# Optimization experiments

Hardware: AMD Instinct MI355X
Metric: run time of the kernel (lower is better)

Reference implementation:

```python
import jax, jax.numpy as jnp
import numpy as np

INPUTDIM = 256
OUTDIM = 256
GRIDSIZE = 300


def setup_inputs() -> dict:
    key = jax.random.key(0)
    k1, k2 = jax.random.split(key)
    x = jax.random.normal(k1, (1024, INPUTDIM), dtype=jnp.float32)
    scale = 1.0 / (np.sqrt(INPUTDIM) * np.sqrt(GRIDSIZE))
    fouriercoeffs = jax.random.normal(k2, (2, OUTDIM, INPUTDIM, GRIDSIZE), dtype=jnp.float32) * scale
    bias = jnp.zeros((1, OUTDIM), dtype=jnp.float32)
    return {"x": x, "fouriercoeffs": fouriercoeffs, "bias": bias}


def reference(x, fouriercoeffs, bias):
    # x: (B, I); fouriercoeffs: (2, O, I, G); bias: (1, O)
    outshape = x.shape[:-1] + (OUTDIM,)
    xf = x.reshape(-1, INPUTDIM)
    k = jnp.arange(1, GRIDSIZE + 1, dtype=xf.dtype)  # (G,)
    phase = xf[:, :, None] * k[None, None, :]        # (B, I, G)
    c = jnp.cos(phase)
    s = jnp.sin(phase)
    y = jnp.einsum('big,jig->bj', c, fouriercoeffs[0]) \
        + jnp.einsum('big,jig->bj', s, fouriercoeffs[1])
    y = y + bias
    return y.reshape(outshape)
```

## Files before the change

kernel.cpp:

```cpp
#include <hip/hip_runtime.h>

#define BATCH   1024
#define IDIM    256
#define ODIM    256
#define GRIDSZ  300

#define BM      128
#define BN      128
#define MT      8
#define NT      2
#define KS_     64
#define IPW     4
#define GS_STEPS 19
#define NSTEPS  (IPW*GS_STEPS)
#define AP      40
#define INV2PI  0.15915494309189535f

typedef __attribute__((ext_vector_type(8))) short  short8;
typedef __attribute__((ext_vector_type(4))) float  f32x4;
typedef __attribute__((ext_vector_type(4))) unsigned int u32x4;

__device__ __forceinline__ unsigned pk(float c, float s) {
  unsigned a = __float_as_uint(c) + 0x8000u;
  unsigned b = __float_as_uint(s) + 0x8000u;
  return __builtin_amdgcn_perm(b, a, 0x07060302u);
}

__device__ __forceinline__ void rot(float& c, float& s, float C, float S) {
  float t1 = s * S;
  float t2 = c * S;
  float cn = __builtin_fmaf(c, C, -t1);
  s = __builtin_fmaf(s, C, t2);
  c = cn;
}

__device__ __forceinline__ void cossin(float rev, float& c, float& s) {
  c = __builtin_amdgcn_cosf(__builtin_amdgcn_fractf(rev));
  s = __builtin_amdgcn_cosf(__builtin_amdgcn_fractf(rev - 0.25f));
}

__global__ void init_out(const float* __restrict__ bias, float* __restrict__ out) {
  const int idx = blockIdx.x * 256 + threadIdx.x;
  out[idx] = bias[idx & (ODIM - 1)];
}

__global__ __launch_bounds__(256, 3) void fkan_gemm(
    const float* __restrict__ x, const float* __restrict__ fc,
    float* __restrict__ out) {
  __shared__ alignas(16) short A_lds[BM * AP];
  __shared__ alignas(16) short B_lds[BN * AP];

  const int tid = threadIdx.x;
  const int id  = blockIdx.x;
  const int z = id & 7, q = id >> 3;
  const int m = q & 7, r = q >> 3;
  const int n  = z & 1;
  const int ks = (z >> 1) | (r << 2);

  const int wave = tid >> 6, lane = tid & 63;
  const int wm = wave >> 1, wn = wave & 1;
  const int fr = lane & 15, fq = lane >> 4;

  const int rA = tid >> 1;
  const int hB = tid & 1;

  const float* xrow = x + (size_t)(m * BM + rA) * IDIM + ks * IPW;
  const float* b0 = fc + ((size_t)(n * BN + rA) * IDIM + ks * IPW) * GRIDSZ + hB * 8;
  const float* b1 = b0 + (size_t)ODIM * IDIM * GRIDSZ;

  short* Awr = &A_lds[rA * AP + hB * 16];
  short* Bwr = &B_lds[rA * AP + hB * 16];
  const short* Ard = &A_lds[(wm * 64 + fr) * AP + fq * 8];
  const short* Brd = &B_lds[(wn * 64 + fr) * AP + fq * 8];

  f32x4 acc[4][4];
#pragma unroll
  for (int a_ = 0; a_ < 4; ++a_)
#pragma unroll
    for (int b_ = 0; b_ < 4; ++b_)
      acc[a_][b_] = (f32x4){0.f, 0.f, 0.f, 0.f};

  float xr = xrow[0] * INV2PI;
  float r1c, r1s, r16c, r16s, sc, ss;
  cossin(xr, r1c, r1s);
  cossin(xr * 16.0f, r16c, r16s);
  cossin(xr * (float)(hB * 8 + 1), sc, ss);
  unsigned ad[8];
  {
    float c = sc, s = ss;
    ad[0] = pk(c, s);
#pragma unroll
    for (int u = 1; u < 8; ++u) { rot(c, s, r1c, r1s); ad[u] = pk(c, s); }
  }
  unsigned bw[8];
  {
    f32x4 L0a = *(const f32x4*)(b0);
    f32x4 L0b = *(const f32x4*)(b0 + 4);
    f32x4 L1a = *(const f32x4*)(b1);
    f32x4 L1b = *(const f32x4*)(b1 + 4);
    bw[0] = pk(L0a.x, L1a.x); bw[1] = pk(L0a.y, L1a.y);
    bw[2] = pk(L0a.z, L1a.z); bw[3] = pk(L0a.w, L1a.w);
    bw[4] = pk(L0b.x, L1b.x); bw[5] = pk(L0b.y, L1b.y);
    bw[6] = pk(L0b.z, L1b.z); bw[7] = pk(L0b.w, L1b.w);
  }

  int il = 0, gs = 0, soff = 0;

  for (int S = 0; S < NSTEPS; ++S) {
    *(u32x4*)Awr       = (u32x4){ad[0], ad[1], ad[2], ad[3]};
    *(u32x4*)(Awr + 8) = (u32x4){ad[4], ad[5], ad[6], ad[7]};
    *(u32x4*)Bwr       = (u32x4){bw[0], bw[1], bw[2], bw[3]};
    *(u32x4*)(Bwr + 8) = (u32x4){bw[4], bw[5], bw[6], bw[7]};
    __syncthreads();

    int gsn = gs + 1, iln = il;
    if (gsn == GS_STEPS) { gsn = 0; iln++; }
    const bool newil = (gsn == 0);
    if (iln >= IPW) iln = 0;
    const int soffn = newil ? iln * GRIDSZ : soff + 16;
    const int o2 = soffn + ((((gsn == 18) ? 1 : 0) & hB) ? 0 : 4);
    f32x4 L0a = *(const f32x4*)(b0 + soffn);
    f32x4 L0b = *(const f32x4*)(b0 + o2);
    f32x4 L1a = *(const f32x4*)(b1 + soffn);
    f32x4 L1b = *(const f32x4*)(b1 + o2);

    short8 aF[4];
#pragma unroll
    for (int tI = 0; tI < 4; ++tI) aF[tI] = *(const short8*)(Ard + tI * 16 * AP);
#pragma unroll
    for (int tJ = 0; tJ < 4; ++tJ) {
      short8 bF = *(const short8*)(Brd + tJ * 16 * AP);
#pragma unroll
      for (int tI = 0; tI < 4; ++tI)
        acc[tI][tJ] = __builtin_amdgcn_mfma_f32_16x16x32_bf16(aF[tI], bF, acc[tI][tJ], 0, 0, 0);
    }

    if (newil) {
      xr = xrow[iln] * INV2PI;
      cossin(xr, r1c, r1s);
      cossin(xr * 16.0f, r16c, r16s);
      cossin(xr * (float)(hB * 8 + 1), sc, ss);
    } else {
      rot(sc, ss, r16c, r16s);
    }
    {
      float c = sc, s = ss;
      ad[0] = pk(c, s);
#pragma unroll
      for (int u = 1; u < 8; ++u) { rot(c, s, r1c, r1s); ad[u] = pk(c, s); }
    }
    if (((gsn == 18) ? 1 : 0) & hB) { ad[4] = 0u; ad[5] = 0u; ad[6] = 0u; ad[7] = 0u; }

    bw[0] = pk(L0a.x, L1a.x); bw[1] = pk(L0a.y, L1a.y);
    bw[2] = pk(L0a.z, L1a.z); bw[3] = pk(L0a.w, L1a.w);
    bw[4] = pk(L0b.x, L1b.x); bw[5] = pk(L0b.y, L1b.y);
    bw[6] = pk(L0b.z, L1b.z); bw[7] = pk(L0b.w, L1b.w);

    il = iln; gs = gsn; soff = soffn;
    __syncthreads();
  }

  const int ob = m * BM + wm * 64 + fq * 4;
  const int oj = n * BN + wn * 64 + fr;
#pragma unroll
  for (int tI = 0; tI < 4; ++tI)
#pragma unroll
    for (int tJ = 0; tJ < 4; ++tJ) {
      float* dst = out + (size_t)(ob + tI * 16) * ODIM + (oj + tJ * 16);
#pragma unroll
      for (int rr = 0; rr < 4; ++rr)
        unsafeAtomicAdd(dst + rr * ODIM, acc[tI][tJ][rr]);
    }
}

extern "C" void kernel_launch(void* const* d_in, const int* in_sizes, int n_in,
                              void* d_out, int out_size, void* d_ws, size_t ws_size,
                              hipStream_t stream) {
  const float* x    = (const float*)d_in[0];
  const float* fc   = (const float*)d_in[1];
  const float* bias = (const float*)d_in[2];
  float* out = (float*)d_out;

  init_out<<<dim3(BATCH * ODIM / 256), dim3(256), 0, stream>>>(bias, out);
  fkan_gemm<<<dim3(MT * NT * KS_), dim3(256), 0, stream>>>(x, fc, out);
}
```

Measured before the change: 367.8 us.

## Halve M tile and double-buffer LDS with a single barrier per step

Shrinks the batch tile from 128 to 64 rows, doubling the grid and halving per-wave accumulators and A-side trig work, with launch bounds raised to 5 blocks per CU. LDS is double-buffered so each step writes the next tile into the other half while MFMAs consume the current one, dropping one of the two barriers per step. The aim is more occupancy and better overlap of global loads and sincos generation with matrix work. In exchange, B-tile loads and output atomics double in total, since each B tile is now shared by fewer batch rows.

```diff
diff --git a/kernel.cpp b/kernel.cpp
--- a/kernel.cpp
+++ b/kernel.cpp
@@ -5,15 +5,17 @@
 #define ODIM    256
 #define GRIDSZ  300
 
-#define BM      128
+#define BM      64
 #define BN      128
-#define MT      8
+#define MT      16
 #define NT      2
 #define KS_     64
 #define IPW     4
 #define GS_STEPS 19
 #define NSTEPS  (IPW*GS_STEPS)
 #define AP      40
+#define B_OFF   2560
+#define HALF_LDS 7680
 #define INV2PI  0.15915494309189535f
 
 typedef __attribute__((ext_vector_type(8))) short  short8;
@@ -44,102 +46,110 @@
   out[idx] = bias[idx & (ODIM - 1)];
 }
 
-__global__ __launch_bounds__(256, 3) void fkan_gemm(
+__global__ __launch_bounds__(256, 5) void fkan_gemm(
     const float* __restrict__ x, const float* __restrict__ fc,
     float* __restrict__ out) {
-  __shared__ alignas(16) short A_lds[BM * AP];
-  __shared__ alignas(16) short B_lds[BN * AP];
+  __shared__ alignas(16) short lds[2 * HALF_LDS];
 
   const int tid = threadIdx.x;
   const int id  = blockIdx.x;
   const int z = id & 7, q = id >> 3;
-  const int m = q & 7, r = q >> 3;
-  const int n  = z & 1;
-  const int ks = (z >> 1) | (r << 2);
+  const int m = q & 15, w = q >> 4;
+  const int c_ = (w << 3) | z;
+  const int ks = c_ >> 1, n = c_ & 1;
 
   const int wave = tid >> 6, lane = tid & 63;
   const int wm = wave >> 1, wn = wave & 1;
   const int fr = lane & 15, fq = lane >> 4;
 
-  const int rA = tid >> 1;
-  const int hB = tid & 1;
+  const int rowA = tid >> 2, q8 = tid & 3;
+  const int rowB = tid >> 1, hB = tid & 1;
 
-  const float* xrow = x + (size_t)(m * BM + rA) * IDIM + ks * IPW;
-  const float* b0 = fc + ((size_t)(n * BN + rA) * IDIM + ks * IPW) * GRIDSZ + hB * 8;
+  const float* xrow = x + (size_t)(m * BM + rowA) * IDIM + ks * IPW;
+  const float* b0 = fc + ((size_t)(n * BN + rowB) * IDIM + ks * IPW) * GRIDSZ;
   const float* b1 = b0 + (size_t)ODIM * IDIM * GRIDSZ;
 
-  short* Awr = &A_lds[rA * AP + hB * 16];
-  short* Bwr = &B_lds[rA * AP + hB * 16];
-  const short* Ard = &A_lds[(wm * 64 + fr) * AP + fq * 8];
-  const short* Brd = &B_lds[(wn * 64 + fr) * AP + fq * 8];
+  const int AwrO = rowA * AP + q8 * 8;
+  const int BwrO = B_OFF + rowB * AP + hB * 16;
+  const int ArdO = (wm * 32 + fr) * AP + fq * 8;
+  const int BrdO = B_OFF + (wn * 64 + fr) * AP + fq * 8;
 
-  f32x4 acc[4][4];
+  f32x4 acc[2][4];
 #pragma unroll
-  for (int a_ = 0; a_ < 4; ++a_)
+  for (int a_ = 0; a_ < 2; ++a_)
 #pragma unroll
     for (int b_ = 0; b_ < 4; ++b_)
       acc[a_][b_] = (f32x4){0.f, 0.f, 0.f, 0.f};
 
-  float xr = xrow[0] * INV2PI;
-  float r1c, r1s, r16c, r16s, sc, ss;
+  float r1c, r1s, r16c, r16s, sc, ss, xr;
+  xr = xrow[0] * INV2PI;
   cossin(xr, r1c, r1s);
-  cossin(xr * 16.0f, r16c, r16s);
-  cossin(xr * (float)(hB * 8 + 1), sc, ss);
-  unsigned ad[8];
+  cossin(16.0f * xr, r16c, r16s);
+  cossin((float)(q8 * 4 + 1) * xr, sc, ss);
+
+  unsigned ad[4];
   {
     float c = sc, s = ss;
     ad[0] = pk(c, s);
 #pragma unroll
-    for (int u = 1; u < 8; ++u) { rot(c, s, r1c, r1s); ad[u] = pk(c, s); }
+    for (int u = 1; u < 4; ++u) { rot(c, s, r1c, r1s); ad[u] = pk(c, s); }
   }
   unsigned bw[8];
   {
-    f32x4 L0a = *(const f32x4*)(b0);
-    f32x4 L0b = *(const f32x4*)(b0 + 4);
-    f32x4 L1a = *(const f32x4*)(b1);
-    f32x4 L1b = *(const f32x4*)(b1 + 4);
+    const int gb = hB * 8;
+    f32x4 L0a = *(const f32x4*)(b0 + gb);
+    f32x4 L0b = *(const f32x4*)(b0 + gb + 4);
+    f32x4 L1a = *(const f32x4*)(b1 + gb);
+    f32x4 L1b = *(const f32x4*)(b1 + gb + 4);
     bw[0] = pk(L0a.x, L1a.x); bw[1] = pk(L0a.y, L1a.y);
     bw[2] = pk(L0a.z, L1a.z); bw[3] = pk(L0a.w, L1a.w);
     bw[4] = pk(L0b.x, L1b.x); bw[5] = pk(L0b.y, L1b.y);
     bw[6] = pk(L0b.z, L1b.z); bw[7] = pk(L0b.w, L1b.w);
   }
+  *(u32x4*)&lds[AwrO]     = (u32x4){ad[0], ad[1], ad[2], ad[3]};
+  *(u32x4*)&lds[BwrO]     = (u32x4){bw[0], bw[1], bw[2], bw[3]};
+  *(u32x4*)&lds[BwrO + 8] = (u32x4){bw[4], bw[5], bw[6], bw[7]};
 
   int il = 0, gs = 0, soff = 0;
 
+#pragma unroll 2
   for (int S = 0; S < NSTEPS; ++S) {
-    *(u32x4*)Awr       = (u32x4){ad[0], ad[1], ad[2], ad[3]};
-    *(u32x4*)(Awr + 8) = (u32x4){ad[4], ad[5], ad[6], ad[7]};
-    *(u32x4*)Bwr       = (u32x4){bw[0], bw[1], bw[2], bw[3]};
-    *(u32x4*)(Bwr + 8) = (u32x4){bw[4], bw[5], bw[6], bw[7]};
+    const short* bufr = lds + (S & 1) * HALF_LDS;
+    short* bufw = lds + ((S + 1) & 1) * HALF_LDS;
     __syncthreads();
 
+    short8 aF0 = *(const short8*)(bufr + ArdO);
+    short8 aF1 = *(const short8*)(bufr + ArdO + 16 * AP);
+    short8 bF0 = *(const short8*)(bufr + BrdO);
+    short8 bF1 = *(const short8*)(bufr + BrdO + 16 * AP);
+    short8 bF2 = *(const short8*)(bufr + BrdO + 32 * AP);
+    short8 bF3 = *(const short8*)(bufr + BrdO + 48 * AP);
+
     int gsn = gs + 1, iln = il;
-    if (gsn == GS_STEPS) { gsn = 0; iln++; }
+    if (gsn == GS_STEPS) { gsn = 0; iln = (il + 1) & (IPW - 1); }
     const bool newil = (gsn == 0);
-    if (iln >= IPW) iln = 0;
     const int soffn = newil ? iln * GRIDSZ : soff + 16;
-    const int o2 = soffn + ((((gsn == 18) ? 1 : 0) & hB) ? 0 : 4);
-    f32x4 L0a = *(const f32x4*)(b0 + soffn);
+    const int gb = soffn + hB * 8;
+    const int o2 = gb + (((gsn == 18) & hB) ? 0 : 4);
+    f32x4 L0a = *(const f32x4*)(b0 + gb);
     f32x4 L0b = *(const f32x4*)(b0 + o2);
-    f32x4 L1a = *(const f32x4*)(b1 + soffn);
+    f32x4 L1a = *(const f32x4*)(b1 + gb);
     f32x4 L1b = *(const f32x4*)(b1 + o2);
 
-    short8 aF[4];
-#pragma unroll
-    for (int tI = 0; tI < 4; ++tI) aF[tI] = *(const short8*)(Ard + tI * 16 * AP);
-#pragma unroll
-    for (int tJ = 0; tJ < 4; ++tJ) {
-      short8 bF = *(const short8*)(Brd + tJ * 16 * AP);
-#pragma unroll
-      for (int tI = 0; tI < 4; ++tI)
-        acc[tI][tJ] = __builtin_amdgcn_mfma_f32_16x16x32_bf16(aF[tI], bF, acc[tI][tJ], 0, 0, 0);
-    }
+    acc[0][0] = __builtin_amdgcn_mfma_f32_16x16x32_bf16(aF0, bF0, acc[0][0], 0, 0, 0);
+    acc[1][0] = __builtin_amdgcn_mfma_f32_16x16x32_bf16(aF1, bF0, acc[1][0], 0, 0, 0);
+    acc[0][1] = __builtin_amdgcn_mfma_f32_16x16x32_bf16(aF0, bF1, acc[0][1], 0, 0, 0);
+    acc[1][1] = __builtin_amdgcn_mfma_f32_16x16x32_bf16(aF1, bF1, acc[1][1], 0, 0, 0);
+    acc[0][2] = __builtin_amdgcn_mfma_f32_16x16x32_bf16(aF0, bF2, acc[0][2], 0, 0, 0);
+    acc[1][2] = __builtin_amdgcn_mfma_f32_16x16x32_bf16(aF1, bF2, acc[1][2], 0, 0, 0);
+    acc[0][3] = __builtin_amdgcn_mfma_f32_16x16x32_bf16(aF0, bF3, acc[0][3], 0, 0, 0);
+    acc[1][3] = __builtin_amdgcn_mfma_f32_16x16x32_bf16(aF1, bF3, acc[1][3], 0, 0, 0);
 
     if (newil) {
       xr = xrow[iln] * INV2PI;
       cossin(xr, r1c, r1s);
-      cossin(xr * 16.0f, r16c, r16s);
-      cossin(xr * (float)(hB * 8 + 1), sc, ss);
+      cossin(16.0f * xr, r16c, r16s);
+      cossin((float)(q8 * 4 + 1) * xr, sc, ss);
     } else {
       rot(sc, ss, r16c, r16s);
     }
@@ -147,23 +157,26 @@
       float c = sc, s = ss;
       ad[0] = pk(c, s);
 #pragma unroll
-      for (int u = 1; u < 8; ++u) { rot(c, s, r1c, r1s); ad[u] = pk(c, s); }
+      for (int u = 1; u < 4; ++u) { rot(c, s, r1c, r1s); ad[u] = pk(c, s); }
     }
-    if (((gsn == 18) ? 1 : 0) & hB) { ad[4] = 0u; ad[5] = 0u; ad[6] = 0u; ad[7] = 0u; }
+    if ((gsn == 18) & (q8 == 3)) { ad[0] = 0u; ad[1] = 0u; ad[2] = 0u; ad[3] = 0u; }
 
     bw[0] = pk(L0a.x, L1a.x); bw[1] = pk(L0a.y, L1a.y);
     bw[2] = pk(L0a.z, L1a.z); bw[3] = pk(L0a.w, L1a.w);
     bw[4] = pk(L0b.x, L1b.x); bw[5] = pk(L0b.y, L1b.y);
     bw[6] = pk(L0b.z, L1b.z); bw[7] = pk(L0b.w, L1b.w);
 
+    *(u32x4*)&bufw[AwrO]     = (u32x4){ad[0], ad[1], ad[2], ad[3]};
+    *(u32x4*)&bufw[BwrO]     = (u32x4){bw[0], bw[1], bw[2], bw[3]};
+    *(u32x4*)&bufw[BwrO + 8] = (u32x4){bw[4], bw[5], bw[6], bw[7]};
+
     il = iln; gs = gsn; soff = soffn;
-    __syncthreads();
   }
 
-  const int ob = m * BM + wm * 64 + fq * 4;
+  const int ob = m * BM + wm * 32 + fq * 4;
   const int oj = n * BN + wn * 64 + fr;
 #pragma unroll
-  for (int tI = 0; tI < 4; ++tI)
+  for (int tI = 0; tI < 2; ++tI)
 #pragma unroll
     for (int tJ = 0; tJ < 4; ++tJ) {
       float* dst = out + (size_t)(ob + tI * 16) * ODIM + (oj + tJ * 16);
```

After: 501.3 us. 36.3% more time.

## Drop LDS staging; each wave builds its own MFMA fragments in registers

Applied to the files above, without the earlier changes.

Replaces the shared-memory staged 128x128 tile GEMM with a register-only scheme. Each wave generates its cos/sin A fragments directly in MFMA layout and loads its B fragments straight from global memory, which removes all LDS traffic and both __syncthreads per step. The block tile becomes 256 (batch) x 64 (out), with each wave owning a 64x64 tile. In exchange, the trig work is duplicated across the waves that share batch rows, and the B loads are narrower per lane and less coalesced, so global-memory efficiency may drop.

```diff
diff --git a/kernel.cpp b/kernel.cpp
--- a/kernel.cpp
+++ b/kernel.cpp
@@ -4,16 +4,9 @@
 #define IDIM    256
 #define ODIM    256
 #define GRIDSZ  300
-
-#define BM      128
-#define BN      128
-#define MT      8
-#define NT      2
 #define KS_     64
 #define IPW     4
-#define GS_STEPS 19
-#define NSTEPS  (IPW*GS_STEPS)
-#define AP      40
+#define CHUNKS  19
 #define INV2PI  0.15915494309189535f
 
 typedef __attribute__((ext_vector_type(8))) short  short8;
@@ -27,8 +20,7 @@
 }
 
 __device__ __forceinline__ void rot(float& c, float& s, float C, float S) {
-  float t1 = s * S;
-  float t2 = c * S;
+  float t1 = s * S, t2 = c * S;
   float cn = __builtin_fmaf(c, C, -t1);
   s = __builtin_fmaf(s, C, t2);
   c = cn;
@@ -44,34 +36,20 @@
   out[idx] = bias[idx & (ODIM - 1)];
 }
 
-__global__ __launch_bounds__(256, 3) void fkan_gemm(
+__global__ __launch_bounds__(256, 3) void fkan(
     const float* __restrict__ x, const float* __restrict__ fc,
     float* __restrict__ out) {
-  __shared__ alignas(16) short A_lds[BM * AP];
-  __shared__ alignas(16) short B_lds[BN * AP];
-
-  const int tid = threadIdx.x;
-  const int id  = blockIdx.x;
-  const int z = id & 7, q = id >> 3;
-  const int m = q & 7, r = q >> 3;
-  const int n  = z & 1;
-  const int ks = (z >> 1) | (r << 2);
+  const int tid = threadIdx.x, id = blockIdx.x;
+  const int z = id & 7;
+  const int m = (id >> 3) & 3;
+  const int nk = (id >> 5) * 8 + z;
+  const int n  = nk & 3;
+  const int ks = nk >> 2;
 
   const int wave = tid >> 6, lane = tid & 63;
-  const int wm = wave >> 1, wn = wave & 1;
   const int fr = lane & 15, fq = lane >> 4;
-
-  const int rA = tid >> 1;
-  const int hB = tid & 1;
-
-  const float* xrow = x + (size_t)(m * BM + rA) * IDIM + ks * IPW;
-  const float* b0 = fc + ((size_t)(n * BN + rA) * IDIM + ks * IPW) * GRIDSZ + hB * 8;
-  const float* b1 = b0 + (size_t)ODIM * IDIM * GRIDSZ;
-
-  short* Awr = &A_lds[rA * AP + hB * 16];
-  short* Bwr = &B_lds[rA * AP + hB * 16];
-  const short* Ard = &A_lds[(wm * 64 + fr) * AP + fq * 8];
-  const short* Brd = &B_lds[(wn * 64 + fr) * AP + fq * 8];
+  const int mbase = m * 256 + wave * 64;
+  const int nbase = n * 64;
 
   f32x4 acc[4][4];
 #pragma unroll
@@ -80,88 +58,76 @@
     for (int b_ = 0; b_ < 4; ++b_)
       acc[a_][b_] = (f32x4){0.f, 0.f, 0.f, 0.f};
 
-  float xr = xrow[0] * INV2PI;
-  float r1c, r1s, r16c, r16s, sc, ss;
-  cossin(xr, r1c, r1s);
-  cossin(xr * 16.0f, r16c, r16s);
-  cossin(xr * (float)(hB * 8 + 1), sc, ss);
-  unsigned ad[8];
-  {
-    float c = sc, s = ss;
-    ad[0] = pk(c, s);
+  float r1c[4], r1s[4], r16c[4], r16s[4], sc_[4], ss_[4];
+  f32x4 B0[4], B1[4];
+  unsigned bF[4][4];
+  int voff[4];
+
+  const float* b1base = fc + (size_t)ODIM * IDIM * GRIDSZ;
+
+#pragma unroll 1
+  for (int il = 0; il < IPW; ++il) {
+    const int i = ks * IPW + il;
 #pragma unroll
-    for (int u = 1; u < 8; ++u) { rot(c, s, r1c, r1s); ad[u] = pk(c, s); }
-  }
-  unsigned bw[8];
-  {
-    f32x4 L0a = *(const f32x4*)(b0);
-    f32x4 L0b = *(const f32x4*)(b0 + 4);
-    f32x4 L1a = *(const f32x4*)(b1);
-    f32x4 L1b = *(const f32x4*)(b1 + 4);
-    bw[0] = pk(L0a.x, L1a.x); bw[1] = pk(L0a.y, L1a.y);
-    bw[2] = pk(L0a.z, L1a.z); bw[3] = pk(L0a.w, L1a.w);
-    bw[4] = pk(L0b.x, L1b.x); bw[5] = pk(L0b.y, L1b.y);
-    bw[6] = pk(L0b.z, L1b.z); bw[7] = pk(L0b.w, L1b.w);
+    for (int tI = 0; tI < 4; ++tI) {
+      float xr = x[(size_t)(mbase + tI * 16 + fr) * IDIM + i] * INV2PI;
+      cossin(xr, r1c[tI], r1s[tI]);
+      cossin(16.0f * xr, r16c[tI], r16s[tI]);
+      cossin((float)(fq * 4 + 1) * xr, sc_[tI], ss_[tI]);
+    }
+#pragma unroll
+    for (int tJ = 0; tJ < 4; ++tJ) {
+      voff[tJ] = ((nbase + tJ * 16 + fr) * IDIM + i) * GRIDSZ + fq * 4;
+      B0[tJ] = *(const f32x4*)(fc + voff[tJ]);
+      B1[tJ] = *(const f32x4*)(b1base + voff[tJ]);
+    }
+
+#pragma unroll 1
+    for (int chunk = 0; chunk < CHUNKS; ++chunk) {
+#pragma unroll
+      for (int tJ = 0; tJ < 4; ++tJ) {
+        bF[tJ][0] = pk(B0[tJ].x, B1[tJ].x);
+        bF[tJ][1] = pk(B0[tJ].y, B1[tJ].y);
+        bF[tJ][2] = pk(B0[tJ].z, B1[tJ].z);
+        bF[tJ][3] = pk(B0[tJ].w, B1[tJ].w);
+      }
+      if (chunk < CHUNKS - 1) {
+        const int sub = ((chunk == CHUNKS - 2) & (fq == 3)) ? 4 : 0;
+#pragma unroll
+        for (int tJ = 0; tJ < 4; ++tJ) {
+          voff[tJ] += 16;
+          const int vu = voff[tJ] - sub;
+          B0[tJ] = *(const f32x4*)(fc + vu);
+          B1[tJ] = *(const f32x4*)(b1base + vu);
+        }
+      }
+      if (chunk == CHUNKS - 1) {
+        if (fq == 3) {
+#pragma unroll
+          for (int tI = 0; tI < 4; ++tI) { sc_[tI] = 0.0f; ss_[tI] = 0.0f; }
+        }
+      }
+#pragma unroll
+      for (int tI = 0; tI < 4; ++tI) {
+        float c = sc_[tI], s = ss_[tI];
+        unsigned a0 = pk(c, s);
+        rot(c, s, r1c[tI], r1s[tI]); unsigned a1 = pk(c, s);
+        rot(c, s, r1c[tI], r1s[tI]); unsigned a2 = pk(c, s);
+        rot(c, s, r1c[tI], r1s[tI]); unsigned a3 = pk(c, s);
+        rot(sc_[tI], ss_[tI], r16c[tI], r16s[tI]);
+        short8 aV = __builtin_bit_cast(short8, (u32x4){a0, a1, a2, a3});
+#pragma unroll
+        for (int tJ = 0; tJ < 4; ++tJ) {
+          short8 bV = __builtin_bit_cast(short8,
+              (u32x4){bF[tJ][0], bF[tJ][1], bF[tJ][2], bF[tJ][3]});
+          acc[tI][tJ] = __builtin_amdgcn_mfma_f32_16x16x32_bf16(aV, bV, acc[tI][tJ], 0, 0, 0);
+        }
+      }
+    }
   }
 
-  int il = 0, gs = 0, soff = 0;
-
-  for (int S = 0; S < NSTEPS; ++S) {
-    *(u32x4*)Awr       = (u32x4){ad[0], ad[1], ad[2], ad[3]};
-    *(u32x4*)(Awr + 8) = (u32x4){ad[4], ad[5], ad[6], ad[7]};
-    *(u32x4*)Bwr       = (u32x4){bw[0], bw[1], bw[2], bw[3]};
-    *(u32x4*)(Bwr + 8) = (u32x4){bw[4], bw[5], bw[6], bw[7]};
-    __syncthreads();
-
-    int gsn = gs + 1, iln = il;
-    if (gsn == GS_STEPS) { gsn = 0; iln++; }
-    const bool newil = (gsn == 0);
-    if (iln >= IPW) iln = 0;
-    const int soffn = newil ? iln * GRIDSZ : soff + 16;
-    const int o2 = soffn + ((((gsn == 18) ? 1 : 0) & hB) ? 0 : 4);
-    f32x4 L0a = *(const f32x4*)(b0 + soffn);
-    f32x4 L0b = *(const f32x4*)(b0 + o2);
-    f32x4 L1a = *(const f32x4*)(b1 + soffn);
-    f32x4 L1b = *(const f32x4*)(b1 + o2);
-
-    short8 aF[4];
-#pragma unroll
-    for (int tI = 0; tI < 4; ++tI) aF[tI] = *(const short8*)(Ard + tI * 16 * AP);
-#pragma unroll
-    for (int tJ = 0; tJ < 4; ++tJ) {
-      short8 bF = *(const short8*)(Brd + tJ * 16 * AP);
-#pragma unroll
-      for (int tI = 0; tI < 4; ++tI)
-        acc[tI][tJ] = __builtin_amdgcn_mfma_f32_16x16x32_bf16(aF[tI], bF, acc[tI][tJ], 0, 0, 0);
-    }
-
-    if (newil) {
-      xr = xrow[iln] * INV2PI;
-      cossin(xr, r1c, r1s);
-      cossin(xr * 16.0f, r16c, r16s);
-      cossin(xr * (float)(hB * 8 + 1), sc, ss);
-    } else {
-      rot(sc, ss, r16c, r16s);
-    }
-    {
-      float c = sc, s = ss;
-      ad[0] = pk(c, s);
-#pragma unroll
-      for (int u = 1; u < 8; ++u) { rot(c, s, r1c, r1s); ad[u] = pk(c, s); }
-    }
-    if (((gsn == 18) ? 1 : 0) & hB) { ad[4] = 0u; ad[5] = 0u; ad[6] = 0u; ad[7] = 0u; }
-
-    bw[0] = pk(L0a.x, L1a.x); bw[1] = pk(L0a.y, L1a.y);
-    bw[2] = pk(L0a.z, L1a.z); bw[3] = pk(L0a.w, L1a.w);
-    bw[4] = pk(L0b.x, L1b.x); bw[5] = pk(L0b.y, L1b.y);
-    bw[6] = pk(L0b.z, L1b.z); bw[7] = pk(L0b.w, L1b.w);
-
-    il = iln; gs = gsn; soff = soffn;
-    __syncthreads();
-  }
-
-  const int ob = m * BM + wm * 64 + fq * 4;
-  const int oj = n * BN + wn * 64 + fr;
+  const int ob = mbase + fq * 4;
+  const int oj = nbase + fr;
 #pragma unroll
   for (int tI = 0; tI < 4; ++tI)
 #pragma unroll
@@ -182,5 +148,5 @@
   float* out = (float*)d_out;
 
   init_out<<<dim3(BATCH * ODIM / 256), dim3(256), 0, stream>>>(bias, out);
-  fkan_gemm<<<dim3(MT * NT * KS_), dim3(256), 0, stream>>>(x, fc, out);
+  fkan<<<dim3(4 * 4 * KS_), dim3(256), 0, stream>>>(x, fc, out);
 }
```

New measurement: 500.1 us. +36.0%, slower.
